# Kernel tuning notes

Measured on AMD Instinct MI355X. Metric: run time of the kernel, lower is better.

The kernel has to match this reference:

```python
import jax, jax.numpy as jnp
import numpy as np

B, T, D, H, V = 512, 40, 300, 200, 50257  # batch, max_length, embed_size, lstm_dimension, vocab
FORGET_BIAS = 1.0  # TF1 LSTMCell default


def setup_inputs() -> dict:
    key = jax.random.key(0)
    ks = jax.random.split(key, 8)
    s = 0.02
    return {
        "input_ids": jax.random.randint(ks[0], (B, T), 0, V, dtype=jnp.int32),
        "lengths": jax.random.randint(ks[1], (B,), 1, T + 1, dtype=jnp.int32),
        "emb": (jax.random.normal(ks[2], (V, D)) * s).astype(jnp.float32),
        "Wx": (jax.random.normal(ks[3], (D, 4 * H)) * s).astype(jnp.float32),
        "Wh": (jax.random.normal(ks[4], (H, 4 * H)) * s).astype(jnp.float32),
        "b": jnp.zeros((4 * H,), jnp.float32),
        "U": (jax.random.normal(ks[5], (H, D)) * s).astype(jnp.float32),
        "b1": jnp.zeros((D,), jnp.float32),
        "b2": jnp.zeros((V,), jnp.float32),
    }


def lstm_last_cell(x, lengths, Wx, Wh, b):
    """TF1 LSTMCell (gate order i, j, f, o; forget_bias=1) unrolled like
    dynamic_rnn with sequence_length: state frozen past each row's length.
    Returns final cell state c of shape [B, H]."""
    Bq = x.shape[0]
    Hq = Wh.shape[0]
    xt = jnp.transpose(x, (1, 0, 2))                      # [T, B, D]
    xproj = xt @ Wx + b                                    # [T, B, 4H] precomputed input GEMM
    tmask = (jnp.arange(x.shape[1])[:, None] < lengths[None, :])[..., None]  # [T, B, 1]

    def step(carry, inp):
        c, h = carry
        xp, m = inp
        gates = xp + h @ Wh                                # [B, 4H]
        i, j, f, o = jnp.split(gates, 4, axis=-1)
        c_new = jax.nn.sigmoid(f + FORGET_BIAS) * c + jax.nn.sigmoid(i) * jnp.tanh(j)
        h_new = jax.nn.sigmoid(o) * jnp.tanh(c_new)
        c = jnp.where(m, c_new, c)
        h = jnp.where(m, h_new, h)
        return (c, h), None

    init = (jnp.zeros((Bq, Hq), x.dtype), jnp.zeros((Bq, Hq), x.dtype))
    (c, _h), _ = jax.lax.scan(step, init, (xproj, tmask))
    return c


def reference(input_ids, lengths, emb, Wx, Wh, b, U, b1, b2):
    x = emb[input_ids]                                     # [B, T, D] embedding lookup
    c = lstm_last_cell(x, lengths, Wx, Wh, b)              # [B, H] final cell state (state.c)
    h1 = jax.nn.relu(c @ U + b1)                           # [B, D]
    # dropout with keep_prob=1 at eval -> identity
    return h1 @ emb.T + b2                                 # [B, V] tied-weight logits
```

## Files before the change

### kernel.cpp

```cpp
#include <hip/hip_runtime.h>
#include <stdint.h>

#define TT_  40
#define HKP_ 224
#define V_   50257
#define VP_  50432

typedef __attribute__((ext_vector_type(4))) float f32x4;
typedef __attribute__((ext_vector_type(8))) short s16x8;

__device__ __forceinline__ ushort bfrn(float f) {
  union { float f; uint32_t u; } x; x.f = f;
  return (ushort)((x.u + 0x7fffu + ((x.u >> 16) & 1u)) >> 16);
}
__device__ __forceinline__ float bl16(uint32_t u) { return __uint_as_float(u << 16); }
__device__ __forceinline__ float bh16(uint32_t u) { return __uint_as_float(u & 0xffff0000u); }
__device__ __forceinline__ float sigm(float x) { return 1.f / (1.f + __expf(-x)); }
__device__ __forceinline__ float tanh_f(float x) { return 1.f - 2.f / (__expf(2.f*x) + 1.f); }

template<int N> struct IC { static constexpr int v = N; };

__global__ void k_prep_emb(const float* __restrict__ emb, ushort* __restrict__ emb_bf) {
  const int idx = blockIdx.x * 256 + threadIdx.x;
  const int v = idx / 80, kc = idx % 80;
  ushort4 o = {0, 0, 0, 0};
  if (v < V_ && kc < 75) {
    const float4 f = *(const float4*)(emb + (size_t)v * 300 + kc * 4);
    o.x = bfrn(f.x); o.y = bfrn(f.y); o.z = bfrn(f.z); o.w = bfrn(f.w);
  }
  *(ushort4*)(emb_bf + (size_t)v * 320 + kc * 4) = o;
}

__global__ void k_prep_small(const float* __restrict__ Wx, const float* __restrict__ Wh,
                             const float* __restrict__ U, ushort* __restrict__ Wxp,
                             ushort* __restrict__ Whp, float* __restrict__ Ut) {
  int idx = blockIdx.x * 256 + threadIdx.x;
  if (idx < 896 * 320) {
    const int colp = idx / 320, k = idx % 320;
    const int n = colp >> 2, g = colp & 3;
    const float v = (colp < 800 && k < 300) ? Wx[(size_t)k * 800 + g * 200 + n] : 0.f;
    Wxp[idx] = bfrn(v);
    return;
  }
  idx -= 896 * 320;
  if (idx < 896 * 224) {
    const int colp = idx / 224, k = idx % 224;
    const int n = colp >> 2, g = colp & 3;
    const float v = (colp < 800 && k < 200) ? Wh[(size_t)k * 800 + g * 200 + n] : 0.f;
    Whp[idx] = bfrn(v);
    return;
  }
  idx -= 896 * 224;
  if (idx < 300 * 200) {
    const int d = idx / 200, h = idx % 200;
    Ut[idx] = U[(size_t)h * 300 + d];
  }
}

__global__ __launch_bounds__(256) void k_xproj(
    const int* __restrict__ ids, const ushort* __restrict__ emb_bf,
    const ushort* __restrict__ Wxp, const float* __restrict__ bias,
    ushort* __restrict__ xp) {
  __shared__ ushort bsm[70 * 512];
  const int tid = threadIdx.x;
  const int w = tid >> 6, lane = tid & 63;
  const int l15 = lane & 15, q = lane >> 4;
  const int wgm = blockIdx.x, wgn = blockIdx.y;
  const int t = wgm >> 3;
  const int bbase = (wgm & 7) << 6;
  const int n0 = wgn * 112;

  for (int s = w; s < 70; s += 4) {
    const int tl = s / 10, kb = s % 10;
    const s16x8 v = *(const s16x8*)(Wxp + (size_t)(n0 + tl * 16 + l15) * 320 + kb * 32 + q * 8);
    *(s16x8*)(&bsm[s * 512 + lane * 8]) = v;
  }
  const int brow = bbase + w * 16 + l15;
  const int id = ids[brow * TT_ + t];
  const ushort* arow = emb_bf + (size_t)id * 320;
  __syncthreads();

  f32x4 acc[7];
  const f32x4 z = {0.f, 0.f, 0.f, 0.f};
#pragma unroll
  for (int tl = 0; tl < 7; ++tl) acc[tl] = z;
  for (int kb = 0; kb < 10; ++kb) {
    const s16x8 af = *(const s16x8*)(arow + kb * 32 + q * 8);
#pragma unroll
    for (int tl = 0; tl < 7; ++tl) {
      const s16x8 bfv = *(const s16x8*)(&bsm[(tl * 10 + kb) * 512 + lane * 8]);
      acc[tl] = __builtin_amdgcn_mfma_f32_16x16x32_bf16(af, bfv, acc[tl], 0, 0, 0);
    }
  }
  const int g16 = ((wgm & 7) << 2) + w;
  ushort* xpb = xp + ((size_t)t * 32 + g16) * 14336;
#pragma unroll
  for (int tl = 0; tl < 7; ++tl) {
    const int colp = n0 + tl * 16 + l15;
    const int T0 = colp >> 4;
    const float bv = (colp < 800) ? bias[(colp & 3) * 200 + (colp >> 2)] : 0.f;
    const int base = T0 * 256 + (l15 >> 2) * 64 + (l15 & 3);
#pragma unroll
    for (int r = 0; r < 4; ++r)
      xpb[base + (q * 4 + r) * 4] = bfrn(acc[tl][r] + bv);
  }
}

__global__ __launch_bounds__(1024)
void k_lstm(
    const ushort* __restrict__ xp, const ushort* __restrict__ Whp,
    const int* __restrict__ lengths, const float* __restrict__ Ut,
    const float* __restrict__ b1v, ushort* __restrict__ h1bf) {
  __shared__ ushort h_lds[2][3584];
  __shared__ ushort wh56_lds[57344];
  __shared__ float  c_lds[16 * 228];

  const int tid = threadIdx.x;
  const int w = tid >> 6, lane = tid & 63;
  const int l15 = lane & 15, q = lane >> 4;
  const int g16 = blockIdx.x;
  const int b0 = g16 << 4;
  const int len = lengths[b0 + l15];
  const bool work = (w < 14);

  s16x8 whf[4][5];
  if (work) {
#pragma unroll
    for (int tl = 0; tl < 4; ++tl) {
      const int T0 = w * 4 + tl;
      const ushort* wr = Whp + (size_t)(T0 * 16 + l15) * HKP_;
#pragma unroll
      for (int kb = 0; kb < 5; ++kb)
        whf[tl][kb] = *(const s16x8*)(wr + kb * 32 + q * 8);
      *(s16x8*)(&wh56_lds[T0 * 1024 + lane * 8])       = *(const s16x8*)(wr + 160 + q * 8);
      *(s16x8*)(&wh56_lds[T0 * 1024 + 512 + lane * 8]) = *(const s16x8*)(wr + 192 + q * 8);
    }
  }
  for (int i = tid; i < 3584; i += 1024) ((uint32_t*)h_lds)[i] = 0;
  for (int i = tid; i < 16 * 228; i += 1024) c_lds[i] = 0.f;

  unsigned nokm = 0;
#pragma unroll
  for (int tl = 0; tl < 4; ++tl) {
    const int n = (w * 4 + tl) * 4 + q;
    if (n < 200) nokm |= (1u << tl);
  }
  const int cidx = l15 * 228 + w * 16 + q;
  const char* xbase = (const char*)xp + ((size_t)g16 * 28672 + (w * 4) * 512 + lane * 8);

  __syncthreads();

  auto step = [&](int t, auto BUFC) {
    constexpr int BUF = decltype(BUFC)::v;
    if (work) {
      const char* xpp = xbase + (size_t)t * (32 * 28672);
      uint2 xv[4];
#pragma unroll
      for (int tl = 0; tl < 4; ++tl) xv[tl] = *(const uint2*)(xpp + tl * 512);

      f32x4 acc[4];
      const f32x4 z = {0.f, 0.f, 0.f, 0.f};
#pragma unroll
      for (int tl = 0; tl < 4; ++tl) acc[tl] = z;
#pragma unroll
      for (int kb = 0; kb < 7; ++kb) {
        const s16x8 hh = *(const s16x8*)(&h_lds[BUF][kb * 512 + lane * 8]);
#pragma unroll
        for (int tl = 0; tl < 4; ++tl) {
          s16x8 a;
          if (kb < 5) a = whf[tl][kb];
          else        a = *(const s16x8*)(&wh56_lds[(w * 4 + tl) * 1024 + (kb - 5) * 512 + lane * 8]);
          acc[tl] = __builtin_amdgcn_mfma_f32_16x16x32_bf16(a, hh, acc[tl], 0, 0, 0);
        }
      }
      const bool act = (t < len);
#pragma unroll
      for (int tl = 0; tl < 4; ++tl) {
        const float g0 = acc[tl][0] + bl16(xv[tl].x);
        const float g1 = acc[tl][1] + bh16(xv[tl].x);
        const float g2 = acc[tl][2] + bl16(xv[tl].y);
        const float g3 = acc[tl][3] + bh16(xv[tl].y);
        const int n = (w * 4 + tl) * 4 + q;
        const int hwoff = (n >> 5) * 1024 + (l15 + (((n >> 3) & 3) << 4)) * 16 + (n & 7) * 2;
        const bool nok = (nokm >> tl) & 1;
        ushort hv = *(const ushort*)((const char*)(&h_lds[BUF][0]) + hwoff);
        if (act && nok) {
          const float cold = c_lds[cidx + 4 * tl];
          const float sf = sigm(g2 + 1.f);
          const float si = sigm(g0);
          const float tj = tanh_f(g1);
          const float cn = sf * cold + si * tj;
          c_lds[cidx + 4 * tl] = cn;
          hv = bfrn(sigm(g3) * tanh_f(cn));
        }
        if (nok)
          *(ushort*)((char*)(&h_lds[BUF ^ 1][0]) + hwoff) = hv;
      }
    }
    __syncthreads();
  };

  for (int tt = 0; tt < TT_ / 2; ++tt) {
    step(2 * tt,     IC<0>{});
    step(2 * tt + 1, IC<1>{});
  }

  for (int i = tid; i < 4800; i += 1024) {
    const int col = i >> 4, row = i & 15;
    const float* ut = Ut + col * 200;
    const float* cr = &c_lds[row * 228];
    float s = 0.f;
    for (int k = 0; k < 200; k += 4) {
      const float4 cc = *(const float4*)(cr + k);
      const float4 uu = *(const float4*)(ut + k);
      s += cc.x * uu.x + cc.y * uu.y + cc.z * uu.z + cc.w * uu.w;
    }
    s += b1v[col];
    h1bf[(size_t)(b0 + row) * 320 + col] = bfrn(fmaxf(s, 0.f));
  }
  if (tid < 320) {
    const int row = tid & 15, col = 300 + (tid >> 4);
    h1bf[(size_t)(b0 + row) * 320 + col] = 0;
  }
}

__global__ __launch_bounds__(256) void k_out(
    const ushort* __restrict__ h1bf, const ushort* __restrict__ emb_bf,
    const float* __restrict__ b2, float* __restrict__ out) {
  const int tid = threadIdx.x;
  const int w = tid >> 6, lane = tid & 63;
  const int l15 = lane & 15, q = lane >> 4;
  const int m0 = blockIdx.y << 6;
  const int n0 = blockIdx.x * 256 + w * 64;
  f32x4 acc[4][4];
  const f32x4 z = {0.f, 0.f, 0.f, 0.f};
#pragma unroll
  for (int a = 0; a < 4; ++a)
#pragma unroll
    for (int b = 0; b < 4; ++b) acc[a][b] = z;
  for (int kb = 0; kb < 10; ++kb) {
    s16x8 af[4], bfv[4];
#pragma unroll
    for (int mt = 0; mt < 4; ++mt)
      af[mt] = *(const s16x8*)(h1bf + (size_t)(m0 + mt * 16 + l15) * 320 + kb * 32 + q * 8);
#pragma unroll
    for (int nt = 0; nt < 4; ++nt)
      bfv[nt] = *(const s16x8*)(emb_bf + (size_t)(n0 + nt * 16 + l15) * 320 + kb * 32 + q * 8);
#pragma unroll
    for (int mt = 0; mt < 4; ++mt)
#pragma unroll
      for (int nt = 0; nt < 4; ++nt)
        acc[mt][nt] = __builtin_amdgcn_mfma_f32_16x16x32_bf16(af[mt], bfv[nt], acc[mt][nt], 0, 0, 0);
  }
#pragma unroll
  for (int nt = 0; nt < 4; ++nt) {
    const int col = n0 + nt * 16 + l15;
    if (col < V_) {
      const float bb = b2[col];
#pragma unroll
      for (int mt = 0; mt < 4; ++mt) {
        const int row = m0 + mt * 16 + q * 4;
#pragma unroll
        for (int r = 0; r < 4; ++r)
          out[(size_t)(row + r) * V_ + col] = acc[mt][nt][r] + bb;
      }
    }
  }
}

extern "C" void kernel_launch(void* const* d_in, const int* in_sizes, int n_in,
                              void* d_out, int out_size, void* d_ws, size_t ws_size,
                              hipStream_t stream) {
  (void)in_sizes; (void)n_in; (void)out_size; (void)ws_size;
  const int*   ids  = (const int*)d_in[0];
  const int*   lens = (const int*)d_in[1];
  const float* emb  = (const float*)d_in[2];
  const float* Wx   = (const float*)d_in[3];
  const float* Wh   = (const float*)d_in[4];
  const float* bg   = (const float*)d_in[5];
  const float* U    = (const float*)d_in[6];
  const float* b1   = (const float*)d_in[7];
  const float* b2   = (const float*)d_in[8];
  float* out = (float*)d_out;

  char* ws = (char*)d_ws;
  ushort* emb_bf = (ushort*)(ws);
  ushort* Wxp    = (ushort*)(ws + 32276480);
  ushort* Whp    = (ushort*)(ws + 32849920);
  float*  Ut     = (float*)(ws + 33251328);
  ushort* h1bf   = (ushort*)(ws + 33491328);
  ushort* xp     = (ushort*)((char*)d_out + 66226176);

  k_prep_emb  <<<15760, 256, 0, stream>>>(emb, emb_bf);
  k_prep_small<<<2139,  256, 0, stream>>>(Wx, Wh, U, Wxp, Whp, Ut);
  k_xproj     <<<dim3(320, 8), 256, 0, stream>>>(ids, emb_bf, Wxp, bg, xp);
  k_lstm      <<<32, 1024, 0, stream>>>(xp, Whp, lens, Ut, b1, h1bf);
  k_out       <<<dim3(197, 8), 256, 0, stream>>>(h1bf, emb_bf, b2, out);
}
```

Baseline: 389.3 us.

## Prefetch next-step xproj, split MFMA accumulators, coalesce xproj stores via LDS

Result: slower. 470.7 us (+20.9%).

```diff
diff --git a/kernel.cpp b/kernel.cpp
--- a/kernel.cpp
+++ b/kernel.cpp
@@ -62,6 +62,7 @@
     const ushort* __restrict__ Wxp, const float* __restrict__ bias,
     ushort* __restrict__ xp) {
   __shared__ ushort bsm[70 * 512];
+  __shared__ ushort xsm[4][1792];
   const int tid = threadIdx.x;
   const int w = tid >> 6, lane = tid & 63;
   const int l15 = lane & 15, q = lane >> 4;
@@ -92,17 +93,21 @@
       acc[tl] = __builtin_amdgcn_mfma_f32_16x16x32_bf16(af, bfv, acc[tl], 0, 0, 0);
     }
   }
+#pragma unroll
+  for (int tl = 0; tl < 7; ++tl) {
+    const int colp = n0 + tl * 16 + l15;
+    const float bv = (colp < 800) ? bias[(colp & 3) * 200 + (colp >> 2)] : 0.f;
+    const int base = tl * 256 + (l15 >> 2) * 64 + (l15 & 3);
+#pragma unroll
+    for (int r = 0; r < 4; ++r)
+      xsm[w][base + (q * 4 + r) * 4] = bfrn(acc[tl][r] + bv);
+  }
   const int g16 = ((wgm & 7) << 2) + w;
   ushort* xpb = xp + ((size_t)t * 32 + g16) * 14336;
 #pragma unroll
   for (int tl = 0; tl < 7; ++tl) {
-    const int colp = n0 + tl * 16 + l15;
-    const int T0 = colp >> 4;
-    const float bv = (colp < 800) ? bias[(colp & 3) * 200 + (colp >> 2)] : 0.f;
-    const int base = T0 * 256 + (l15 >> 2) * 64 + (l15 & 3);
-#pragma unroll
-    for (int r = 0; r < 4; ++r)
-      xpb[base + (q * 4 + r) * 4] = bfrn(acc[tl][r] + bv);
+    const ushort4 vv = *(const ushort4*)(&xsm[w][tl * 256 + lane * 4]);
+    *(ushort4*)(xpb + (size_t)(wgn * 7 + tl) * 256 + lane * 4) = vv;
   }
 }
 
@@ -148,20 +153,25 @@
   const int cidx = l15 * 228 + w * 16 + q;
   const char* xbase = (const char*)xp + ((size_t)g16 * 28672 + (w * 4) * 512 + lane * 8);
 
+  uint2 xva[4], xvb[4];
+  if (work) {
+#pragma unroll
+    for (int tl = 0; tl < 4; ++tl) xva[tl] = *(const uint2*)(xbase + tl * 512);
+  }
   __syncthreads();
 
-  auto step = [&](int t, auto BUFC) {
+  auto step = [&](int t, auto BUFC, uint2* xcur, uint2* xnext) {
     constexpr int BUF = decltype(BUFC)::v;
     if (work) {
-      const char* xpp = xbase + (size_t)t * (32 * 28672);
-      uint2 xv[4];
-#pragma unroll
-      for (int tl = 0; tl < 4; ++tl) xv[tl] = *(const uint2*)(xpp + tl * 512);
-
-      f32x4 acc[4];
+      if (t + 1 < TT_) {
+        const char* xpp = xbase + (size_t)(t + 1) * (32 * 28672);
+#pragma unroll
+        for (int tl = 0; tl < 4; ++tl) xnext[tl] = *(const uint2*)(xpp + tl * 512);
+      }
+      f32x4 accA[4], accB[4];
       const f32x4 z = {0.f, 0.f, 0.f, 0.f};
 #pragma unroll
-      for (int tl = 0; tl < 4; ++tl) acc[tl] = z;
+      for (int tl = 0; tl < 4; ++tl) { accA[tl] = z; accB[tl] = z; }
 #pragma unroll
       for (int kb = 0; kb < 7; ++kb) {
         const s16x8 hh = *(const s16x8*)(&h_lds[BUF][kb * 512 + lane * 8]);
@@ -170,16 +180,18 @@
           s16x8 a;
           if (kb < 5) a = whf[tl][kb];
           else        a = *(const s16x8*)(&wh56_lds[(w * 4 + tl) * 1024 + (kb - 5) * 512 + lane * 8]);
-          acc[tl] = __builtin_amdgcn_mfma_f32_16x16x32_bf16(a, hh, acc[tl], 0, 0, 0);
+          if (kb & 1) accB[tl] = __builtin_amdgcn_mfma_f32_16x16x32_bf16(a, hh, accB[tl], 0, 0, 0);
+          else        accA[tl] = __builtin_amdgcn_mfma_f32_16x16x32_bf16(a, hh, accA[tl], 0, 0, 0);
         }
       }
       const bool act = (t < len);
 #pragma unroll
       for (int tl = 0; tl < 4; ++tl) {
-        const float g0 = acc[tl][0] + bl16(xv[tl].x);
-        const float g1 = acc[tl][1] + bh16(xv[tl].x);
-        const float g2 = acc[tl][2] + bl16(xv[tl].y);
-        const float g3 = acc[tl][3] + bh16(xv[tl].y);
+        const f32x4 gs = accA[tl] + accB[tl];
+        const float g0 = gs[0] + bl16(xcur[tl].x);
+        const float g1 = gs[1] + bh16(xcur[tl].x);
+        const float g2 = gs[2] + bl16(xcur[tl].y);
+        const float g3 = gs[3] + bh16(xcur[tl].y);
         const int n = (w * 4 + tl) * 4 + q;
         const int hwoff = (n >> 5) * 1024 + (l15 + (((n >> 3) & 3) << 4)) * 16 + (n & 7) * 2;
         const bool nok = (nokm >> tl) & 1;
@@ -197,12 +209,12 @@
           *(ushort*)((char*)(&h_lds[BUF ^ 1][0]) + hwoff) = hv;
       }
     }
-    __syncthreads();
+    asm volatile("s_waitcnt lgkmcnt(0)\n\ts_barrier" ::: "memory");
   };
 
   for (int tt = 0; tt < TT_ / 2; ++tt) {
-    step(2 * tt,     IC<0>{});
-    step(2 * tt + 1, IC<1>{});
+    step(2 * tt,     IC<0>{}, xva, xvb);
+    step(2 * tt + 1, IC<1>{}, xvb, xva);
   }
 
   for (int i = tid; i < 4800; i += 1024) {
```

## Fuse input projection into LSTM recurrence and stream weights from global

Applied to the files above, without the earlier changes.

Result: slower. 1.231 ms (+216.2%).

```diff
diff --git a/kernel.cpp b/kernel.cpp
--- a/kernel.cpp
+++ b/kernel.cpp
@@ -13,8 +13,6 @@
   union { float f; uint32_t u; } x; x.f = f;
   return (ushort)((x.u + 0x7fffu + ((x.u >> 16) & 1u)) >> 16);
 }
-__device__ __forceinline__ float bl16(uint32_t u) { return __uint_as_float(u << 16); }
-__device__ __forceinline__ float bh16(uint32_t u) { return __uint_as_float(u & 0xffff0000u); }
 __device__ __forceinline__ float sigm(float x) { return 1.f / (1.f + __expf(-x)); }
 __device__ __forceinline__ float tanh_f(float x) { return 1.f - 2.f / (__expf(2.f*x) + 1.f); }
 
@@ -57,63 +55,16 @@
   }
 }
 
-__global__ __launch_bounds__(256) void k_xproj(
-    const int* __restrict__ ids, const ushort* __restrict__ emb_bf,
-    const ushort* __restrict__ Wxp, const float* __restrict__ bias,
-    ushort* __restrict__ xp) {
-  __shared__ ushort bsm[70 * 512];
-  const int tid = threadIdx.x;
-  const int w = tid >> 6, lane = tid & 63;
-  const int l15 = lane & 15, q = lane >> 4;
-  const int wgm = blockIdx.x, wgn = blockIdx.y;
-  const int t = wgm >> 3;
-  const int bbase = (wgm & 7) << 6;
-  const int n0 = wgn * 112;
-
-  for (int s = w; s < 70; s += 4) {
-    const int tl = s / 10, kb = s % 10;
-    const s16x8 v = *(const s16x8*)(Wxp + (size_t)(n0 + tl * 16 + l15) * 320 + kb * 32 + q * 8);
-    *(s16x8*)(&bsm[s * 512 + lane * 8]) = v;
-  }
-  const int brow = bbase + w * 16 + l15;
-  const int id = ids[brow * TT_ + t];
-  const ushort* arow = emb_bf + (size_t)id * 320;
-  __syncthreads();
-
-  f32x4 acc[7];
-  const f32x4 z = {0.f, 0.f, 0.f, 0.f};
-#pragma unroll
-  for (int tl = 0; tl < 7; ++tl) acc[tl] = z;
-  for (int kb = 0; kb < 10; ++kb) {
-    const s16x8 af = *(const s16x8*)(arow + kb * 32 + q * 8);
-#pragma unroll
-    for (int tl = 0; tl < 7; ++tl) {
-      const s16x8 bfv = *(const s16x8*)(&bsm[(tl * 10 + kb) * 512 + lane * 8]);
-      acc[tl] = __builtin_amdgcn_mfma_f32_16x16x32_bf16(af, bfv, acc[tl], 0, 0, 0);
-    }
-  }
-  const int g16 = ((wgm & 7) << 2) + w;
-  ushort* xpb = xp + ((size_t)t * 32 + g16) * 14336;
-#pragma unroll
-  for (int tl = 0; tl < 7; ++tl) {
-    const int colp = n0 + tl * 16 + l15;
-    const int T0 = colp >> 4;
-    const float bv = (colp < 800) ? bias[(colp & 3) * 200 + (colp >> 2)] : 0.f;
-    const int base = T0 * 256 + (l15 >> 2) * 64 + (l15 & 3);
-#pragma unroll
-    for (int r = 0; r < 4; ++r)
-      xpb[base + (q * 4 + r) * 4] = bfrn(acc[tl][r] + bv);
-  }
-}
-
 __global__ __launch_bounds__(1024)
 void k_lstm(
-    const ushort* __restrict__ xp, const ushort* __restrict__ Whp,
-    const int* __restrict__ lengths, const float* __restrict__ Ut,
-    const float* __restrict__ b1v, ushort* __restrict__ h1bf) {
+    const int* __restrict__ ids, const ushort* __restrict__ emb_bf,
+    const ushort* __restrict__ Wxp, const ushort* __restrict__ Whp,
+    const int* __restrict__ lengths, const float* __restrict__ bg,
+    const float* __restrict__ Ut, const float* __restrict__ b1v,
+    ushort* __restrict__ h1bf) {
   __shared__ ushort h_lds[2][3584];
-  __shared__ ushort wh56_lds[57344];
   __shared__ float  c_lds[16 * 228];
+  __shared__ float  bb_lds[4 * 224];
 
   const int tid = threadIdx.x;
   const int w = tid >> 6, lane = tid & 63;
@@ -123,78 +74,97 @@
   const int len = lengths[b0 + l15];
   const bool work = (w < 14);
 
-  s16x8 whf[4][5];
-  if (work) {
-#pragma unroll
-    for (int tl = 0; tl < 4; ++tl) {
-      const int T0 = w * 4 + tl;
-      const ushort* wr = Whp + (size_t)(T0 * 16 + l15) * HKP_;
-#pragma unroll
-      for (int kb = 0; kb < 5; ++kb)
-        whf[tl][kb] = *(const s16x8*)(wr + kb * 32 + q * 8);
-      *(s16x8*)(&wh56_lds[T0 * 1024 + lane * 8])       = *(const s16x8*)(wr + 160 + q * 8);
-      *(s16x8*)(&wh56_lds[T0 * 1024 + 512 + lane * 8]) = *(const s16x8*)(wr + 192 + q * 8);
-    }
+  for (int i = tid; i < 896; i += 1024) {
+    const int g = i / 224, n = i % 224;
+    bb_lds[i] = (n < 200) ? bg[g * 200 + n] : 0.f;
   }
   for (int i = tid; i < 3584; i += 1024) ((uint32_t*)h_lds)[i] = 0;
-  for (int i = tid; i < 16 * 228; i += 1024) c_lds[i] = 0.f;
-
+
+  const ushort* whb[4];
+  const ushort* wxb[4];
+  int hwoff[4], nn[4];
   unsigned nokm = 0;
 #pragma unroll
   for (int tl = 0; tl < 4; ++tl) {
-    const int n = (w * 4 + tl) * 4 + q;
+    const int T0 = w * 4 + tl;
+    whb[tl] = Whp + (size_t)(T0 * 16 + l15) * HKP_ + q * 8;
+    wxb[tl] = Wxp + (size_t)(T0 * 16 + l15) * 320 + q * 8;
+    const int n = T0 * 4 + q;
+    nn[tl] = n;
     if (n < 200) nokm |= (1u << tl);
-  }
-  const int cidx = l15 * 228 + w * 16 + q;
-  const char* xbase = (const char*)xp + ((size_t)g16 * 28672 + (w * 4) * 512 + lane * 8);
-
+    hwoff[tl] = (n >> 5) * 1024 + (l15 + (((n >> 3) & 3) << 4)) * 16 + (n & 7) * 2;
+  }
+  float  cr[4] = {0.f, 0.f, 0.f, 0.f};
+  ushort hr[4] = {0, 0, 0, 0};
+
+  const int* idrow = ids + (size_t)(b0 + l15) * TT_;
+  int idc = idrow[0];
   __syncthreads();
 
   auto step = [&](int t, auto BUFC) {
     constexpr int BUF = decltype(BUFC)::v;
     if (work) {
-      const char* xpp = xbase + (size_t)t * (32 * 28672);
-      uint2 xv[4];
-#pragma unroll
-      for (int tl = 0; tl < 4; ++tl) xv[tl] = *(const uint2*)(xpp + tl * 512);
-
+      const ushort* xrow = emb_bf + (size_t)idc * 320 + q * 8;
+      s16x8 xf[2], wx[2][4];
+      xf[0] = *(const s16x8*)(xrow);
+      xf[1] = *(const s16x8*)(xrow + 32);
+#pragma unroll
+      for (int tl = 0; tl < 4; ++tl) {
+        wx[0][tl] = *(const s16x8*)(wxb[tl]);
+        wx[1][tl] = *(const s16x8*)(wxb[tl] + 32);
+      }
+      idc = idrow[t + 1 < TT_ ? t + 1 : TT_ - 1];
       f32x4 acc[4];
       const f32x4 z = {0.f, 0.f, 0.f, 0.f};
 #pragma unroll
       for (int tl = 0; tl < 4; ++tl) acc[tl] = z;
+      s16x8 hh[2], wh[2][4];
+      hh[0] = *(const s16x8*)(&h_lds[BUF][lane * 8]);
+#pragma unroll
+      for (int tl = 0; tl < 4; ++tl) wh[0][tl] = *(const s16x8*)(whb[tl]);
 #pragma unroll
       for (int kb = 0; kb < 7; ++kb) {
-        const s16x8 hh = *(const s16x8*)(&h_lds[BUF][kb * 512 + lane * 8]);
-#pragma unroll
-        for (int tl = 0; tl < 4; ++tl) {
-          s16x8 a;
-          if (kb < 5) a = whf[tl][kb];
-          else        a = *(const s16x8*)(&wh56_lds[(w * 4 + tl) * 1024 + (kb - 5) * 512 + lane * 8]);
-          acc[tl] = __builtin_amdgcn_mfma_f32_16x16x32_bf16(a, hh, acc[tl], 0, 0, 0);
+        if (kb + 1 < 7) {
+          hh[(kb + 1) & 1] = *(const s16x8*)(&h_lds[BUF][(kb + 1) * 512 + lane * 8]);
+#pragma unroll
+          for (int tl = 0; tl < 4; ++tl)
+            wh[(kb + 1) & 1][tl] = *(const s16x8*)(whb[tl] + (kb + 1) * 32);
         }
+#pragma unroll
+        for (int tl = 0; tl < 4; ++tl)
+          acc[tl] = __builtin_amdgcn_mfma_f32_16x16x32_bf16(wh[kb & 1][tl], hh[kb & 1], acc[tl], 0, 0, 0);
+      }
+#pragma unroll
+      for (int kb = 0; kb < 10; ++kb) {
+#pragma unroll
+        for (int tl = 0; tl < 4; ++tl)
+          acc[tl] = __builtin_amdgcn_mfma_f32_16x16x32_bf16(wx[kb & 1][tl], xf[kb & 1], acc[tl], 0, 0, 0);
+        if (kb + 2 < 10) {
+          xf[kb & 1] = *(const s16x8*)(xrow + (kb + 2) * 32);
+#pragma unroll
+          for (int tl = 0; tl < 4; ++tl)
+            wx[kb & 1][tl] = *(const s16x8*)(wxb[tl] + (kb + 2) * 32);
+        }
       }
       const bool act = (t < len);
 #pragma unroll
       for (int tl = 0; tl < 4; ++tl) {
-        const float g0 = acc[tl][0] + bl16(xv[tl].x);
-        const float g1 = acc[tl][1] + bh16(xv[tl].x);
-        const float g2 = acc[tl][2] + bl16(xv[tl].y);
-        const float g3 = acc[tl][3] + bh16(xv[tl].y);
-        const int n = (w * 4 + tl) * 4 + q;
-        const int hwoff = (n >> 5) * 1024 + (l15 + (((n >> 3) & 3) << 4)) * 16 + (n & 7) * 2;
+        const int n = nn[tl];
+        const float g0 = acc[tl][0] + bb_lds[n];
+        const float g1 = acc[tl][1] + bb_lds[224 + n];
+        const float g2 = acc[tl][2] + bb_lds[448 + n];
+        const float g3 = acc[tl][3] + bb_lds[672 + n];
         const bool nok = (nokm >> tl) & 1;
-        ushort hv = *(const ushort*)((const char*)(&h_lds[BUF][0]) + hwoff);
         if (act && nok) {
-          const float cold = c_lds[cidx + 4 * tl];
           const float sf = sigm(g2 + 1.f);
           const float si = sigm(g0);
           const float tj = tanh_f(g1);
-          const float cn = sf * cold + si * tj;
-          c_lds[cidx + 4 * tl] = cn;
-          hv = bfrn(sigm(g3) * tanh_f(cn));
+          const float cn = sf * cr[tl] + si * tj;
+          cr[tl] = cn;
+          hr[tl] = bfrn(sigm(g3) * tanh_f(cn));
         }
         if (nok)
-          *(ushort*)((char*)(&h_lds[BUF ^ 1][0]) + hwoff) = hv;
+          *(ushort*)((char*)(&h_lds[BUF ^ 1][0]) + hwoff[tl]) = hr[tl];
       }
     }
     __syncthreads();
@@ -205,15 +175,22 @@
     step(2 * tt + 1, IC<1>{});
   }
 
+  if (work) {
+#pragma unroll
+    for (int tl = 0; tl < 4; ++tl)
+      if ((nokm >> tl) & 1) c_lds[l15 * 228 + nn[tl]] = cr[tl];
+  }
+  __syncthreads();
+
   for (int i = tid; i < 4800; i += 1024) {
     const int col = i >> 4, row = i & 15;
     const float* ut = Ut + col * 200;
-    const float* cr = &c_lds[row * 228];
+    const float* cc_ = &c_lds[row * 228];
     float s = 0.f;
     for (int k = 0; k < 200; k += 4) {
-      const float4 cc = *(const float4*)(cr + k);
+      const float4 cv = *(const float4*)(cc_ + k);
       const float4 uu = *(const float4*)(ut + k);
-      s += cc.x * uu.x + cc.y * uu.y + cc.z * uu.z + cc.w * uu.w;
+      s += cv.x * uu.x + cv.y * uu.y + cv.z * uu.z + cv.w * uu.w;
     }
     s += b1v[col];
     h1bf[(size_t)(b0 + row) * 320 + col] = bfrn(fmaxf(s, 0.f));
@@ -289,11 +266,9 @@
   ushort* Whp    = (ushort*)(ws + 32849920);
   float*  Ut     = (float*)(ws + 33251328);
   ushort* h1bf   = (ushort*)(ws + 33491328);
-  ushort* xp     = (ushort*)((char*)d_out + 66226176);
 
   k_prep_emb  <<<15760, 256, 0, stream>>>(emb, emb_bf);
   k_prep_small<<<2139,  256, 0, stream>>>(Wx, Wh, U, Wxp, Whp, Ut);
-  k_xproj     <<<dim3(320, 8), 256, 0, stream>>>(ids, emb_bf, Wxp, bg, xp);
-  k_lstm      <<<32, 1024, 0, stream>>>(xp, Whp, lens, Ut, b1, h1bf);
+  k_lstm      <<<32, 1024, 0, stream>>>(ids, emb_bf, Wxp, Whp, lens, bg, Ut, b1, h1bf);
   k_out       <<<dim3(197, 8), 256, 0, stream>>>(h1bf, emb_bf, b2, out);
 }
```
